# Kernel tuning notes

Hardware: AMD Instinct MI355X
Metric: run time of the kernel (lower is better)

## Reference

```python
import jax, jax.numpy as jnp
import numpy as np

EMBED_DIM = 128
NUM_HEADS = 4
WIN = (7, 7)
N = WIN[0] * WIN[1]  # 49
NW = 64              # windows per image
B = 128              # batch of images
SCALE = (EMBED_DIM // NUM_HEADS) ** -0.5


def _relative_position_index():
    coords = np.stack(np.meshgrid(np.arange(WIN[0]), np.arange(WIN[1]), indexing='ij'))
    cf = coords.reshape(2, -1)                       # [2, N]
    rel = cf[:, :, None] - cf[:, None, :]            # [2, N, N]
    rel = rel.transpose(1, 2, 0).astype(np.int64)    # [N, N, 2]
    rel[..., 0] += WIN[0] - 1
    rel[..., 0] *= 2 * WIN[1] - 1
    rel[..., 1] += WIN[1] - 1
    return rel.sum(-1).reshape(-1)                   # [N*N]


def setup_inputs() -> dict:
    key = jax.random.key(0)
    ks = jax.random.split(key, 6)
    C = EMBED_DIM
    x = jax.random.normal(ks[0], (NW * B, N, C), dtype=jnp.float32)
    mask = jnp.zeros((NW, N, N), dtype=jnp.float32)
    qkv_w = jax.random.normal(ks[1], (3 * C, C), dtype=jnp.float32) * (C ** -0.5)
    qkv_b = jnp.zeros((3 * C,), dtype=jnp.float32)
    proj_w = jax.random.normal(ks[2], (C, C), dtype=jnp.float32) * (C ** -0.5)
    proj_b = jnp.zeros((C,), dtype=jnp.float32)
    bias_table = jax.random.normal(ks[3], ((2 * WIN[0] - 1) * (2 * WIN[1] - 1), NUM_HEADS), dtype=jnp.float32) * 0.02
    rel_index = jnp.asarray(_relative_position_index(), dtype=jnp.int32)
    return {"x": x, "mask": mask, "qkv_w": qkv_w, "qkv_b": qkv_b,
            "proj_w": proj_w, "proj_b": proj_b, "bias_table": bias_table,
            "rel_index": rel_index}


def reference(x, mask, qkv_w, qkv_b, proj_w, proj_b, bias_table, rel_index):
    nwb, n, c = x.shape
    nh, ch = NUM_HEADS, c // NUM_HEADS
    qkv = x @ qkv_w.T + qkv_b                               # [nwb, n, 3c]
    qkv = qkv.reshape(nwb, n, 3, nh, ch)
    q, k, v = (jnp.moveaxis(qkv, (2, 3), (0, 2))[i] for i in range(3))  # each [nwb, nh, n, ch]
    attn = jnp.einsum('whik,whjk->whij', q * SCALE, k)      # [nwb, nh, n, n]
    # relative position bias: gather then reshape to [1, nh, n, n]
    bias = bias_table[rel_index].reshape(n, n, nh).transpose(2, 0, 1)[None]
    attn = attn + bias
    if mask is not None:
        nw = mask.shape[0]
        attn = attn.reshape(nwb // nw, nw, nh, n, n) + mask[None, :, None]
        attn = attn.reshape(nwb, nh, n, n)
    attn = jax.nn.softmax(attn, axis=-1)
    out = jnp.einsum('whij,whjd->whid', attn, v)            # [nwb, nh, n, ch]
    out = out.transpose(0, 2, 1, 3).reshape(nwb, n, c)
    return out @ proj_w.T + proj_b
```

## Files before the change

kernel.cpp:

```cpp
#include <hip/hip_runtime.h>

typedef __bf16 bf16x8 __attribute__((ext_vector_type(8)));
typedef __bf16 bf16x4 __attribute__((ext_vector_type(4)));
typedef float  f32x4  __attribute__((ext_vector_type(4)));

#define NTOK  49
#define CDIM  128
#define LOG2E 1.4426950408889634f
#define QK2   (0.17677669529663687f * LOG2E)

#define WQKV_OFF  0
#define WPROJ_OFF 98304
#define BIASB_OFF 131072
#define MASKB_OFF 163840

__device__ __forceinline__ int swz(int row, int col) {
    return (col & ~63) | ((((col >> 3) ^ row) & 7) << 3) | (col & 7);
}

__global__ void prep_kernel(const float* __restrict__ qkv_w,
                            const float* __restrict__ proj_w,
                            const float* __restrict__ bias_table,
                            const int*   __restrict__ rel_index,
                            const float* __restrict__ mask,
                            __bf16* __restrict__ wqkv,
                            __bf16* __restrict__ wproj,
                            __bf16* __restrict__ biasb,
                            __bf16* __restrict__ maskb) {
    int t = blockIdx.x * 256 + threadIdx.x;
    if (t < 384 * 128) wqkv[t]  = (__bf16)qkv_w[t];
    if (t < 128 * 128) wproj[t] = (__bf16)proj_w[t];
    if (t < 4096) {
        int base = t * 4;
        int h = base >> 12, i = (base >> 6) & 63, j0 = base & 63;
        bf16x4 v;
        #pragma unroll
        for (int r = 0; r < 4; ++r) {
            int j = j0 + r;
            float f = 0.f;
            if (i < NTOK && j < NTOK) f = bias_table[rel_index[i*49 + j] * 4 + h] * LOG2E;
            v[r] = (__bf16)f;
        }
        *(bf16x4*)&biasb[base] = v;
    }
    {
        int base = t * 4;
        int wm = base >> 12, i = (base >> 6) & 63, j0 = base & 63;
        bf16x4 v;
        #pragma unroll
        for (int r = 0; r < 4; ++r) {
            int j = j0 + r;
            float f;
            if (j >= NTOK)      f = -1e30f;
            else if (i < NTOK)  f = mask[wm*2401 + i*49 + j] * LOG2E;
            else                f = 0.f;
            v[r] = (__bf16)f;
        }
        *(bf16x4*)&maskb[base] = v;
    }
}

__launch_bounds__(256, 3)
__global__ void winattn_kernel(const float* __restrict__ x,
                               const float* __restrict__ qkv_b,
                               const float* __restrict__ proj_b,
                               const __bf16* __restrict__ wqkv,
                               const __bf16* __restrict__ wproj,
                               const __bf16* __restrict__ biasb,
                               const __bf16* __restrict__ maskb,
                               float* __restrict__ out) {
    __shared__ __bf16 lds_a[64 * 128];
    __shared__ __bf16 lds_b[64 * 256];

    const int tid  = threadIdx.x;
    const int w    = blockIdx.x;
    const int wave = tid >> 6;
    const int lane = tid & 63;
    const int quad = lane >> 4;
    const int l16  = lane & 15;

    {
        int row = tid >> 2;
        int c0  = (tid & 3) * 32;
        __align__(16) __bf16 tmp[32];
        if (row < NTOK) {
            const float4* src = (const float4*)(x + ((size_t)w * NTOK + row) * CDIM + c0);
            #pragma unroll
            for (int i = 0; i < 8; ++i) {
                float4 f = src[i];
                tmp[i*4+0] = (__bf16)f.x; tmp[i*4+1] = (__bf16)f.y;
                tmp[i*4+2] = (__bf16)f.z; tmp[i*4+3] = (__bf16)f.w;
            }
        } else {
            #pragma unroll
            for (int i = 0; i < 32; ++i) tmp[i] = (__bf16)0.0f;
        }
        #pragma unroll
        for (int i = 0; i < 4; ++i)
            *(bf16x8*)&lds_a[row * 128 + swz(row, c0 + i*8)] = *(bf16x8*)&tmp[i*8];
    }
    __syncthreads();

    bf16x4 vreg[2][4];
    #pragma unroll
    for (int half = 0; half < 2; ++half) {
        const int tq = half*4 + wave;
        const int tk = wave*2 + half;
        const int tv = half*4 + wave;
        f32x4 aq[4], ak[4], av[4];
        #pragma unroll
        for (int m = 0; m < 4; ++m) {
            aq[m] = (f32x4){0.f,0.f,0.f,0.f};
            ak[m] = (f32x4){0.f,0.f,0.f,0.f};
            av[m] = (f32x4){0.f,0.f,0.f,0.f};
        }
        #pragma unroll
        for (int kt = 0; kt < 4; ++kt) {
            bf16x8 xf[4];
            #pragma unroll
            for (int mt = 0; mt < 4; ++mt) {
                int rr = mt*16 + l16;
                xf[mt] = *(bf16x8*)&lds_a[rr * 128 + swz(rr, kt*32 + quad*8)];
            }
            bf16x8 wq = *(const bf16x8*)(wqkv + (size_t)(      tq*16 + l16) * CDIM + kt*32 + quad*8);
            bf16x8 wk = *(const bf16x8*)(wqkv + (size_t)(128 + tk*16 + l16) * CDIM + kt*32 + quad*8);
            bf16x8 wv = *(const bf16x8*)(wqkv + (size_t)(256 + tv*16 + l16) * CDIM + kt*32 + quad*8);
            #pragma unroll
            for (int mt = 0; mt < 4; ++mt) {
                aq[mt] = __builtin_amdgcn_mfma_f32_16x16x32_bf16(wq, xf[mt], aq[mt], 0, 0, 0);
                ak[mt] = __builtin_amdgcn_mfma_f32_16x16x32_bf16(wk, xf[mt], ak[mt], 0, 0, 0);
                av[mt] = __builtin_amdgcn_mfma_f32_16x16x32_bf16(xf[mt], wv, av[mt], 0, 0, 0);
            }
        }
        float4 bq4 = *(const float4*)&qkv_b[      tq*16 + quad*4];
        float4 bk4 = *(const float4*)&qkv_b[128 + tk*16 + quad*4];
        float  bv1 = qkv_b[256 + tv*16 + l16];
        #pragma unroll
        for (int mt = 0; mt < 4; ++mt) {
            int row = mt*16 + l16;
            bf16x4 qv, kv, vv;
            #pragma unroll
            for (int r = 0; r < 4; ++r) {
                qv[r] = (__bf16)((aq[mt][r] + ((const float*)&bq4)[r]) * QK2);
                kv[r] = (__bf16)( ak[mt][r] + ((const float*)&bk4)[r]);
                vv[r] = (__bf16)( av[mt][r] + bv1);
            }
            *(bf16x4*)&lds_b[row*256 + swz(row,       tq*16 + quad*4)] = qv;
            *(bf16x4*)&lds_b[row*256 + swz(row, 128 + tk*16 + quad*4)] = kv;
            vreg[half][mt] = vv;
        }
    }
    __syncthreads();

    #pragma unroll
    for (int half = 0; half < 2; ++half) {
        int vc = (half*4 + wave)*16 + l16;
        #pragma unroll
        for (int mt = 0; mt < 4; ++mt)
            *(bf16x4*)&lds_a[vc * 64 + swz(vc, mt*16 + quad*4)] = vreg[half][mt];
    }

    const int h = wave;
    float inv[4];
    {
        bf16x8 kf[4], qf[4];
        #pragma unroll
        for (int t = 0; t < 4; ++t) {
            int rr = t*16 + l16;
            kf[t] = *(bf16x8*)&lds_b[rr*256 + swz(rr, 128 + h*32 + quad*8)];
            qf[t] = *(bf16x8*)&lds_b[rr*256 + swz(rr,       h*32 + quad*8)];
        }
        __syncthreads();

        f32x4 s2[4][4];
        #pragma unroll
        for (int mtq = 0; mtq < 4; ++mtq)
            #pragma unroll
            for (int ntk = 0; ntk < 4; ++ntk) {
                f32x4 z = (f32x4){0.f,0.f,0.f,0.f};
                s2[mtq][ntk] = __builtin_amdgcn_mfma_f32_16x16x32_bf16(kf[ntk], qf[mtq], z, 0, 0, 0);
            }

        const __bf16* bb = biasb + h * 4096;
        const __bf16* mb = maskb + (size_t)(w & 63) * 4096;
        #pragma unroll
        for (int mtq = 0; mtq < 4; ++mtq) {
            int i = mtq*16 + l16;
            float e[4][4], sum = 0.f;
            #pragma unroll
            for (int ntk = 0; ntk < 4; ++ntk) {
                int j0 = ntk*16 + quad*4;
                bf16x4 b4 = *(const bf16x4*)&bb[i*64 + j0];
                bf16x4 m4 = *(const bf16x4*)&mb[i*64 + j0];
                #pragma unroll
                for (int r = 0; r < 4; ++r) {
                    float t = s2[mtq][ntk][r] + (float)b4[r] + (float)m4[r];
                    e[ntk][r] = __builtin_amdgcn_exp2f(t);
                    sum += e[ntk][r];
                }
            }
            sum += __shfl_xor(sum, 16, 64);
            sum += __shfl_xor(sum, 32, 64);
            inv[mtq] = __builtin_amdgcn_rcpf(sum);
            #pragma unroll
            for (int ntk = 0; ntk < 4; ++ntk) {
                bf16x4 pv;
                #pragma unroll
                for (int r = 0; r < 4; ++r) pv[r] = (__bf16)e[ntk][r];
                *(bf16x4*)&lds_b[h*4096 + i*64 + swz(i, ntk*16 + quad*4)] = pv;
            }
        }
    }

    {
        bf16x8 vf[2][2];
        #pragma unroll
        for (int nv = 0; nv < 2; ++nv)
            #pragma unroll
            for (int kt = 0; kt < 2; ++kt) {
                int vr = h*32 + nv*16 + l16;
                vf[nv][kt] = *(bf16x8*)&lds_a[vr*64 + swz(vr, kt*32 + quad*8)];
            }
        bf16x8 pf[4][2];
        #pragma unroll
        for (int mtq = 0; mtq < 4; ++mtq)
            #pragma unroll
            for (int kt = 0; kt < 2; ++kt) {
                int pr = mtq*16 + l16;
                pf[mtq][kt] = *(bf16x8*)&lds_b[h*4096 + pr*64 + swz(pr, kt*32 + quad*8)];
            }
        __syncthreads();

        f32x4 oacc[2][4];
        #pragma unroll
        for (int a = 0; a < 2; ++a)
            #pragma unroll
            for (int b = 0; b < 4; ++b) oacc[a][b] = (f32x4){0.f,0.f,0.f,0.f};
        #pragma unroll
        for (int mtq = 0; mtq < 4; ++mtq)
            #pragma unroll
            for (int kt = 0; kt < 2; ++kt)
                #pragma unroll
                for (int nv = 0; nv < 2; ++nv)
                    oacc[nv][mtq] = __builtin_amdgcn_mfma_f32_16x16x32_bf16(
                        vf[nv][kt], pf[mtq][kt], oacc[nv][mtq], 0, 0, 0);

        #pragma unroll
        for (int nv = 0; nv < 2; ++nv)
            #pragma unroll
            for (int mtq = 0; mtq < 4; ++mtq) {
                int row = mtq*16 + l16;
                bf16x4 ov;
                #pragma unroll
                for (int r = 0; r < 4; ++r) ov[r] = (__bf16)(oacc[nv][mtq][r] * inv[mtq]);
                *(bf16x4*)&lds_b[row*128 + swz(row, h*32 + nv*16 + quad*4)] = ov;
            }
    }
    __syncthreads();

    #pragma unroll
    for (int ntl = 0; ntl < 2; ++ntl) {
        int oc = (wave*2 + ntl) * 16;
        f32x4 acc[4];
        #pragma unroll
        for (int a = 0; a < 4; ++a) acc[a] = (f32x4){0.f,0.f,0.f,0.f};
        #pragma unroll
        for (int kt = 0; kt < 4; ++kt) {
            bf16x8 wf = *(const bf16x8*)(wproj + (size_t)(oc + l16) * CDIM + kt*32 + quad*8);
            #pragma unroll
            for (int mt = 0; mt < 4; ++mt) {
                int rr = mt*16 + l16;
                bf16x8 of = *(bf16x8*)&lds_b[rr*128 + swz(rr, kt*32 + quad*8)];
                acc[mt] = __builtin_amdgcn_mfma_f32_16x16x32_bf16(wf, of, acc[mt], 0, 0, 0);
            }
        }
        float4 pb4 = *(const float4*)&proj_b[oc + quad*4];
        #pragma unroll
        for (int mt = 0; mt < 4; ++mt) {
            int tok = mt*16 + l16;
            if (tok < NTOK) {
                float4 o4;
                o4.x = acc[mt][0] + pb4.x;
                o4.y = acc[mt][1] + pb4.y;
                o4.z = acc[mt][2] + pb4.z;
                o4.w = acc[mt][3] + pb4.w;
                *(float4*)&out[((size_t)w * NTOK + tok) * CDIM + oc + quad*4] = o4;
            }
        }
    }
}

extern "C" void kernel_launch(void* const* d_in, const int* in_sizes, int n_in,
                              void* d_out, int out_size, void* d_ws, size_t ws_size,
                              hipStream_t stream) {
    const float* x          = (const float*)d_in[0];
    const float* mask       = (const float*)d_in[1];
    const float* qkv_w      = (const float*)d_in[2];
    const float* qkv_b      = (const float*)d_in[3];
    const float* proj_w     = (const float*)d_in[4];
    const float* proj_b     = (const float*)d_in[5];
    const float* bias_table = (const float*)d_in[6];
    const int*   rel_index  = (const int*)d_in[7];

    __bf16* wqkv  = (__bf16*)((char*)d_ws + WQKV_OFF);
    __bf16* wproj = (__bf16*)((char*)d_ws + WPROJ_OFF);
    __bf16* biasb = (__bf16*)((char*)d_ws + BIASB_OFF);
    __bf16* maskb = (__bf16*)((char*)d_ws + MASKB_OFF);

    int nwb = in_sizes[0] / (NTOK * CDIM);

    prep_kernel<<<256, 256, 0, stream>>>(qkv_w, proj_w, bias_table, rel_index, mask,
                                         wqkv, wproj, biasb, maskb);
    winattn_kernel<<<nwb, 256, 0, stream>>>(x, qkv_b, proj_b,
                                            wqkv, wproj, biasb, maskb, (float*)d_out);
}
```

Baseline: 543.7 us.

## Permute QKV weight rows so Q/K/P stay in registers, cut LDS

```diff
diff --git a/kernel.cpp b/kernel.cpp
--- a/kernel.cpp
+++ b/kernel.cpp
@@ -28,7 +28,20 @@
                             __bf16* __restrict__ biasb,
                             __bf16* __restrict__ maskb) {
     int t = blockIdx.x * 256 + threadIdx.x;
-    if (t < 384 * 128) wqkv[t]  = (__bf16)qkv_w[t];
+    if (t < 384 * 128) {
+        int row = t >> 7, c = t & 127;
+        int orow;
+        if (row < 256) {
+            int sec = row >> 7;
+            int h   = (row & 127) >> 5;
+            int w5  = row & 31;
+            int half = w5 >> 4, l = w5 & 15;
+            orow = sec * 128 + h * 32 + ((l >> 2) << 3) + half * 4 + (l & 3);
+        } else {
+            orow = row;
+        }
+        wqkv[t] = (__bf16)qkv_w[orow * 128 + c];
+    }
     if (t < 128 * 128) wproj[t] = (__bf16)proj_w[t];
     if (t < 4096) {
         int base = t * 4;
@@ -60,7 +73,7 @@
     }
 }
 
-__launch_bounds__(256, 3)
+__launch_bounds__(256, 4)
 __global__ void winattn_kernel(const float* __restrict__ x,
                                const float* __restrict__ qkv_b,
                                const float* __restrict__ proj_b,
@@ -69,12 +82,12 @@
                                const __bf16* __restrict__ biasb,
                                const __bf16* __restrict__ maskb,
                                float* __restrict__ out) {
-    __shared__ __bf16 lds_a[64 * 128];
-    __shared__ __bf16 lds_b[64 * 256];
+    __shared__ __bf16 lds_xv[64 * 128];
+    __shared__ __bf16 lds_o [64 * 128];
 
     const int tid  = threadIdx.x;
     const int w    = blockIdx.x;
-    const int wave = tid >> 6;
+    const int h    = tid >> 6;
     const int lane = tid & 63;
     const int quad = lane >> 4;
     const int l16  = lane & 15;
@@ -97,16 +110,14 @@
         }
         #pragma unroll
         for (int i = 0; i < 4; ++i)
-            *(bf16x8*)&lds_a[row * 128 + swz(row, c0 + i*8)] = *(bf16x8*)&tmp[i*8];
+            *(bf16x8*)&lds_xv[row * 128 + swz(row, c0 + i*8)] = *(bf16x8*)&tmp[i*8];
     }
     __syncthreads();
 
+    bf16x8 qf[4], kf[4];
     bf16x4 vreg[2][4];
     #pragma unroll
     for (int half = 0; half < 2; ++half) {
-        const int tq = half*4 + wave;
-        const int tk = wave*2 + half;
-        const int tv = half*4 + wave;
         f32x4 aq[4], ak[4], av[4];
         #pragma unroll
         for (int m = 0; m < 4; ++m) {
@@ -120,11 +131,12 @@
             #pragma unroll
             for (int mt = 0; mt < 4; ++mt) {
                 int rr = mt*16 + l16;
-                xf[mt] = *(bf16x8*)&lds_a[rr * 128 + swz(rr, kt*32 + quad*8)];
-            }
-            bf16x8 wq = *(const bf16x8*)(wqkv + (size_t)(      tq*16 + l16) * CDIM + kt*32 + quad*8);
-            bf16x8 wk = *(const bf16x8*)(wqkv + (size_t)(128 + tk*16 + l16) * CDIM + kt*32 + quad*8);
-            bf16x8 wv = *(const bf16x8*)(wqkv + (size_t)(256 + tv*16 + l16) * CDIM + kt*32 + quad*8);
+                xf[mt] = *(bf16x8*)&lds_xv[rr * 128 + swz(rr, kt*32 + quad*8)];
+            }
+            size_t ro = (size_t)(h*32 + half*16 + l16) * CDIM + kt*32 + quad*8;
+            bf16x8 wq = *(const bf16x8*)(wqkv + ro);
+            bf16x8 wk = *(const bf16x8*)(wqkv + 128*CDIM + ro);
+            bf16x8 wv = *(const bf16x8*)(wqkv + 256*CDIM + ro);
             #pragma unroll
             for (int mt = 0; mt < 4; ++mt) {
                 aq[mt] = __builtin_amdgcn_mfma_f32_16x16x32_bf16(wq, xf[mt], aq[mt], 0, 0, 0);
@@ -132,21 +144,19 @@
                 av[mt] = __builtin_amdgcn_mfma_f32_16x16x32_bf16(xf[mt], wv, av[mt], 0, 0, 0);
             }
         }
-        float4 bq4 = *(const float4*)&qkv_b[      tq*16 + quad*4];
-        float4 bk4 = *(const float4*)&qkv_b[128 + tk*16 + quad*4];
-        float  bv1 = qkv_b[256 + tv*16 + l16];
+        float4 bq4 = *(const float4*)&qkv_b[      h*32 + quad*8 + half*4];
+        float4 bk4 = *(const float4*)&qkv_b[128 + h*32 + quad*8 + half*4];
+        float  bv1 = qkv_b[256 + h*32 + half*16 + l16];
         #pragma unroll
         for (int mt = 0; mt < 4; ++mt) {
-            int row = mt*16 + l16;
-            bf16x4 qv, kv, vv;
             #pragma unroll
             for (int r = 0; r < 4; ++r) {
-                qv[r] = (__bf16)((aq[mt][r] + ((const float*)&bq4)[r]) * QK2);
-                kv[r] = (__bf16)( ak[mt][r] + ((const float*)&bk4)[r]);
-                vv[r] = (__bf16)( av[mt][r] + bv1);
-            }
-            *(bf16x4*)&lds_b[row*256 + swz(row,       tq*16 + quad*4)] = qv;
-            *(bf16x4*)&lds_b[row*256 + swz(row, 128 + tk*16 + quad*4)] = kv;
+                qf[mt][half*4+r] = (__bf16)((aq[mt][r] + ((const float*)&bq4)[r]) * QK2);
+                kf[mt][half*4+r] = (__bf16)( ak[mt][r] + ((const float*)&bk4)[r]);
+            }
+            bf16x4 vv;
+            #pragma unroll
+            for (int r = 0; r < 4; ++r) vv[r] = (__bf16)(av[mt][r] + bv1);
             vreg[half][mt] = vv;
         }
     }
@@ -154,37 +164,27 @@
 
     #pragma unroll
     for (int half = 0; half < 2; ++half) {
-        int vc = (half*4 + wave)*16 + l16;
-        #pragma unroll
-        for (int mt = 0; mt < 4; ++mt)
-            *(bf16x4*)&lds_a[vc * 64 + swz(vc, mt*16 + quad*4)] = vreg[half][mt];
-    }
-
-    const int h = wave;
+        int vc = h*32 + half*16 + l16;
+        #pragma unroll
+        for (int mt = 0; mt < 4; ++mt) {
+            int col = (mt >> 1)*32 + quad*8 + (mt & 1)*4;
+            *(bf16x4*)&lds_xv[vc * 64 + swz(vc, col)] = vreg[half][mt];
+        }
+    }
+
+    bf16x8 pf[4][2];
     float inv[4];
     {
-        bf16x8 kf[4], qf[4];
-        #pragma unroll
-        for (int t = 0; t < 4; ++t) {
-            int rr = t*16 + l16;
-            kf[t] = *(bf16x8*)&lds_b[rr*256 + swz(rr, 128 + h*32 + quad*8)];
-            qf[t] = *(bf16x8*)&lds_b[rr*256 + swz(rr,       h*32 + quad*8)];
-        }
-        __syncthreads();
-
-        f32x4 s2[4][4];
-        #pragma unroll
-        for (int mtq = 0; mtq < 4; ++mtq)
+        const __bf16* bb = biasb + h * 4096;
+        const __bf16* mb = maskb + (size_t)(w & 63) * 4096;
+        #pragma unroll
+        for (int mtq = 0; mtq < 4; ++mtq) {
+            f32x4 s2[4];
             #pragma unroll
             for (int ntk = 0; ntk < 4; ++ntk) {
                 f32x4 z = (f32x4){0.f,0.f,0.f,0.f};
-                s2[mtq][ntk] = __builtin_amdgcn_mfma_f32_16x16x32_bf16(kf[ntk], qf[mtq], z, 0, 0, 0);
-            }
-
-        const __bf16* bb = biasb + h * 4096;
-        const __bf16* mb = maskb + (size_t)(w & 63) * 4096;
-        #pragma unroll
-        for (int mtq = 0; mtq < 4; ++mtq) {
+                s2[ntk] = __builtin_amdgcn_mfma_f32_16x16x32_bf16(kf[ntk], qf[mtq], z, 0, 0, 0);
+            }
             int i = mtq*16 + l16;
             float e[4][4], sum = 0.f;
             #pragma unroll
@@ -194,7 +194,7 @@
                 bf16x4 m4 = *(const bf16x4*)&mb[i*64 + j0];
                 #pragma unroll
                 for (int r = 0; r < 4; ++r) {
-                    float t = s2[mtq][ntk][r] + (float)b4[r] + (float)m4[r];
+                    float t = s2[ntk][r] + (float)b4[r] + (float)m4[r];
                     e[ntk][r] = __builtin_amdgcn_exp2f(t);
                     sum += e[ntk][r];
                 }
@@ -203,11 +203,14 @@
             sum += __shfl_xor(sum, 32, 64);
             inv[mtq] = __builtin_amdgcn_rcpf(sum);
             #pragma unroll
-            for (int ntk = 0; ntk < 4; ++ntk) {
-                bf16x4 pv;
+            for (int kt = 0; kt < 2; ++kt) {
+                bf16x8 p8;
                 #pragma unroll
-                for (int r = 0; r < 4; ++r) pv[r] = (__bf16)e[ntk][r];
-                *(bf16x4*)&lds_b[h*4096 + i*64 + swz(i, ntk*16 + quad*4)] = pv;
+                for (int b = 0; b < 2; ++b)
+                    #pragma unroll
+                    for (int r = 0; r < 4; ++r)
+                        p8[b*4+r] = (__bf16)e[2*kt+b][r];
+                pf[mtq][kt] = p8;
             }
         }
     }
@@ -219,18 +222,8 @@
             #pragma unroll
             for (int kt = 0; kt < 2; ++kt) {
                 int vr = h*32 + nv*16 + l16;
-                vf[nv][kt] = *(bf16x8*)&lds_a[vr*64 + swz(vr, kt*32 + quad*8)];
-            }
-        bf16x8 pf[4][2];
-        #pragma unroll
-        for (int mtq = 0; mtq < 4; ++mtq)
-            #pragma unroll
-            for (int kt = 0; kt < 2; ++kt) {
-                int pr = mtq*16 + l16;
-                pf[mtq][kt] = *(bf16x8*)&lds_b[h*4096 + pr*64 + swz(pr, kt*32 + quad*8)];
-            }
-        __syncthreads();
-
+                vf[nv][kt] = *(bf16x8*)&lds_xv[vr*64 + swz(vr, kt*32 + quad*8)];
+            }
         f32x4 oacc[2][4];
         #pragma unroll
         for (int a = 0; a < 2; ++a)
@@ -253,14 +246,14 @@
                 bf16x4 ov;
                 #pragma unroll
                 for (int r = 0; r < 4; ++r) ov[r] = (__bf16)(oacc[nv][mtq][r] * inv[mtq]);
-                *(bf16x4*)&lds_b[row*128 + swz(row, h*32 + nv*16 + quad*4)] = ov;
+                *(bf16x4*)&lds_o[row*128 + swz(row, h*32 + nv*16 + quad*4)] = ov;
             }
     }
     __syncthreads();
 
     #pragma unroll
     for (int ntl = 0; ntl < 2; ++ntl) {
-        int oc = (wave*2 + ntl) * 16;
+        int oc = (h*2 + ntl) * 16;
         f32x4 acc[4];
         #pragma unroll
         for (int a = 0; a < 4; ++a) acc[a] = (f32x4){0.f,0.f,0.f,0.f};
@@ -270,7 +263,7 @@
             #pragma unroll
             for (int mt = 0; mt < 4; ++mt) {
                 int rr = mt*16 + l16;
-                bf16x8 of = *(bf16x8*)&lds_b[rr*128 + swz(rr, kt*32 + quad*8)];
+                bf16x8 of = *(bf16x8*)&lds_o[rr*128 + swz(rr, kt*32 + quad*8)];
                 acc[mt] = __builtin_amdgcn_mfma_f32_16x16x32_bf16(wf, of, acc[mt], 0, 0, 0);
             }
         }
```

After: 791.0 us. 45.5% more time.
